# Kernel optimization log

Measured on AMD Instinct MI355X. Metric: run time of the kernel, lower is better.

## Reference

```python
import jax, jax.numpy as jnp
import numpy as np

D_EMB = 1024
N_HEADS = 16
HEAD_DIM = D_EMB // N_HEADS


def _xavier(key, out_f, in_f):
    limit = jnp.sqrt(6.0 / (in_f + out_f))
    return jax.random.uniform(key, (out_f, in_f), jnp.float32, -limit, limit)


def setup_inputs() -> dict:
    key = jax.random.key(0)
    k_x, k_qkv, k_out = jax.random.split(key, 3)
    x = jax.random.normal(k_x, (4, 2048, D_EMB), jnp.float32)
    # torch nn.Linear weights: [out_features, in_features], xavier_uniform; biases zero
    w_qkv = _xavier(k_qkv, 3 * D_EMB, D_EMB)
    b_qkv = jnp.zeros((3 * D_EMB,), jnp.float32)
    w_out = _xavier(k_out, D_EMB, D_EMB)
    b_out = jnp.zeros((D_EMB,), jnp.float32)
    return {"x": x, "w_qkv": w_qkv, "b_qkv": b_qkv, "w_out": w_out, "b_out": b_out}


def reference(x, w_qkv, b_qkv, w_out, b_out):
    B, S, D = x.shape
    # QKV projection: y = x @ W^T + b -> [B, S, 3D]
    qkv = jnp.einsum('bsd,ed->bse', x, w_qkv) + b_qkv
    # view(B, S, H, 3*head_dim) then split into q, k, v (matches torch chunk on last dim)
    qkv = qkv.reshape(B, S, N_HEADS, 3 * HEAD_DIM)
    q, k, v = jnp.split(qkv, 3, axis=-1)  # each [B, S, H, head_dim]
    scale = 1.0 / jnp.sqrt(jnp.float32(HEAD_DIM))
    scores = jnp.einsum('bshd,bthd->bhst', q, k) * scale  # [B, H, S, S]
    probs = jax.nn.softmax(scores, axis=-1)
    out = jnp.einsum('bhst,bthd->bshd', probs, v).reshape(B, S, D)
    return jnp.einsum('bsd,ed->bse', out, w_out) + b_out
```

## Files before the change

### kernel.cpp

```cpp
#include <hip/hip_runtime.h>

typedef __bf16 bf16_t;
typedef __bf16 bf16x8 __attribute__((ext_vector_type(8)));
typedef __bf16 bf16x4 __attribute__((ext_vector_type(4)));
typedef float f32x4 __attribute__((ext_vector_type(4)));

#define S_LEN 2048
#define D_EMB 1024
#define NH 16

#define MFMA16(a, b, c) __builtin_amdgcn_mfma_f32_16x16x32_bf16((a), (b), (c), 0, 0, 0)

__device__ __forceinline__ void gld16(void* lds, const void* g) {
  __builtin_amdgcn_global_load_lds(
      (__attribute__((address_space(1))) void*)(void*)(g),
      (__attribute__((address_space(3))) void*)(lds), 16, 0, 0);
}

__device__ __forceinline__ float exp2_hw(float x) {
  float r;
  asm("v_exp_f32 %0, %1" : "=v"(r) : "v"(x));
  return r;
}

__global__ __launch_bounds__(256) void cvt_bf16(const float* __restrict__ in,
                                                bf16_t* __restrict__ out, int n4) {
  int i = blockIdx.x * 256 + threadIdx.x;
  if (i >= n4) return;
  float4 v = ((const float4*)in)[i];
  bf16x4 o;
  o[0] = (bf16_t)v.x; o[1] = (bf16_t)v.y; o[2] = (bf16_t)v.z; o[3] = (bf16_t)v.w;
  ((bf16x4*)out)[i] = o;
}

template <int EPI>
__global__ __launch_bounds__(256) void gemm_bt(
    const bf16_t* __restrict__ A, const bf16_t* __restrict__ W,
    const float* __restrict__ bias, float* __restrict__ outF,
    bf16_t* __restrict__ outQ, int M, int N, int K) {
  __shared__ __attribute__((aligned(16))) bf16_t As[128 * 64];
  __shared__ __attribute__((aligned(16))) bf16_t Ws[128 * 64];
  const int tid = threadIdx.x;
  const int lane = tid & 63;
  const int wid = tid >> 6;
  const int l15 = lane & 15, lg = lane >> 4;
  int lin = blockIdx.x + gridDim.x * blockIdx.y;
  const int nwg = gridDim.x * gridDim.y;
  lin = (lin & 7) * (nwg >> 3) + (lin >> 3);
  const int tm = (lin / gridDim.x) * 128, tn = (lin % gridDim.x) * 128;
  const int wm = (wid >> 1) * 64, wn = (wid & 1) * 64;
  f32x4 acc[4][4] = {};
  const int q0 = tid * 16;

  for (int k0 = 0; k0 < K; k0 += 64) {
#pragma unroll
    for (int i = 0; i < 4; ++i) {
      int q = q0 + i * 4096;
      int row = q >> 7;
      int scb = (q & 127) ^ ((row & 7) << 4);
      gld16((char*)As + (q & ~1023),
            (const char*)A + ((size_t)(tm + row) * K + k0) * 2 + scb);
      gld16((char*)Ws + (q & ~1023),
            (const char*)W + ((size_t)(tn + row) * K + k0) * 2 + scb);
    }
    __syncthreads();
#pragma unroll
    for (int kk = 0; kk < 2; ++kk) {
      const int cb = kk * 64 + lg * 16;
      bf16x8 af[4], bfr[4];
#pragma unroll
      for (int mi = 0; mi < 4; ++mi) {
        int row = wm + mi * 16 + l15;
        af[mi] = *(const bf16x8*)((const char*)As + row * 128 + (cb ^ ((row & 7) << 4)));
      }
#pragma unroll
      for (int ni = 0; ni < 4; ++ni) {
        int row = wn + ni * 16 + l15;
        bfr[ni] = *(const bf16x8*)((const char*)Ws + row * 128 + (cb ^ ((row & 7) << 4)));
      }
#pragma unroll
      for (int mi = 0; mi < 4; ++mi)
#pragma unroll
        for (int ni = 0; ni < 4; ++ni)
          acc[mi][ni] = MFMA16(af[mi], bfr[ni], acc[mi][ni]);
    }
    __syncthreads();
  }

  if (EPI == 0) {
#pragma unroll
    for (int mi = 0; mi < 4; ++mi)
#pragma unroll
      for (int ni = 0; ni < 4; ++ni) {
        int colg = tn + wn + ni * 16 + l15;
        float bv = bias[colg];
#pragma unroll
        for (int j = 0; j < 4; ++j) {
          int rowg = tm + wm + mi * 16 + lg * 4 + j;
          outF[(size_t)rowg * N + colg] = acc[mi][ni][j] + bv;
        }
      }
  } else {
#pragma unroll
    for (int mi = 0; mi < 4; ++mi)
#pragma unroll
      for (int ni = 0; ni < 4; ++ni) {
        int e = tn + wn + ni * 16 + l15;
        float bv = bias[e];
        int h = e / 192;
        int r = e - h * 192;
        int t = r >> 6, c = r & 63;
#pragma unroll
        for (int j = 0; j < 4; ++j) {
          int m = tm + wm + mi * 16 + lg * 4 + j;
          int b = m >> 11, s = m & 2047;
          float v = acc[mi][ni][j] + bv;
          if (t == 0) v *= 0.18033688011112042f;
          size_t base = ((size_t)(b * NH + h) * 3 + t) * (size_t)(S_LEN * 64);
          size_t idx;
          if (t == 2) {
            int rs = s & 31;
            int rp = (((rs >> 2) & 3) << 3) | ((rs >> 4) << 2) | (rs & 3);
            idx = base + (size_t)c * S_LEN + (size_t)((s & ~31) | rp);
          } else {
            idx = base + (size_t)s * 64 + c;
          }
          outQ[idx] = (bf16_t)v;
        }
      }
  }
}

__global__ __launch_bounds__(256) void attn_fwd(const bf16_t* __restrict__ qkvb,
                                                bf16_t* __restrict__ attnb) {
  __shared__ __attribute__((aligned(16))) bf16_t Ks[2][64 * 64];
  __shared__ __attribute__((aligned(16))) bf16_t Vs[2][64 * 64];
  const int tid = threadIdx.x, lane = tid & 63, wid = tid >> 6;
  const int l15 = lane & 15, lg = lane >> 4;
  int lin = blockIdx.x + (blockIdx.y << 4);
  lin = (lin & 7) * 128 + (lin >> 3);
  const int qt = lin & 15;
  const int bh = lin >> 4;
  const int b = bh >> 4, h = bh & 15;
  const char* Qg = (const char*)qkvb + (size_t)bh * 3 * (S_LEN * 64) * 2;
  const char* Kg = Qg + (size_t)S_LEN * 64 * 2;
  const char* Vtg = Kg + (size_t)S_LEN * 64 * 2;
  const int q0 = tid * 16;

#pragma unroll
  for (int i = 0; i < 2; ++i) {
    int q = q0 + i * 4096;
    int row = q >> 7;
    int scb = (q & 127) ^ ((row & 7) << 4);
    gld16((char*)Ks[0] + (q & ~1023), Kg + (size_t)row * 128 + scb);
    gld16((char*)Vs[0] + (q & ~1023), Vtg + (size_t)row * (S_LEN * 2) + scb);
  }

  bf16x8 qf[2][2];
#pragma unroll
  for (int mi = 0; mi < 2; ++mi) {
    const char* qr = Qg + (size_t)(qt * 128 + wid * 32 + mi * 16 + l15) * 128;
#pragma unroll
    for (int kb = 0; kb < 2; ++kb)
      qf[mi][kb] = *(const bf16x8*)(qr + kb * 64 + lg * 16);
  }
  __syncthreads();

  float lsum[2] = {0.f, 0.f};
  f32x4 o[2][4] = {};
  const int swk = (l15 & 7) << 4;

  for (int kt = 0; kt < 32; ++kt) {
    const int cur = kt & 1;
    if (kt < 31) {
#pragma unroll
      for (int i = 0; i < 2; ++i) {
        int q = q0 + i * 4096;
        int row = q >> 7;
        int scb = (q & 127) ^ ((row & 7) << 4);
        gld16((char*)Ks[cur ^ 1] + (q & ~1023),
              Kg + (size_t)((kt + 1) * 64 + row) * 128 + scb);
        gld16((char*)Vs[cur ^ 1] + (q & ~1023),
              Vtg + (size_t)row * (S_LEN * 2) + (kt + 1) * 128 + scb);
      }
    }

    f32x4 stv[2][4];
#pragma unroll
    for (int nk = 0; nk < 4; ++nk) {
      const char* kr = (const char*)Ks[cur] + (nk * 16 + l15) * 128;
      bf16x8 kf0 = *(const bf16x8*)(kr + ((lg * 16) ^ swk));
      bf16x8 kf1 = *(const bf16x8*)(kr + ((64 + lg * 16) ^ swk));
#pragma unroll
      for (int mi = 0; mi < 2; ++mi) {
        f32x4 z = {};
        z = MFMA16(kf0, qf[mi][0], z);
        stv[mi][nk] = MFMA16(kf1, qf[mi][1], z);
      }
    }

#pragma unroll
    for (int mi = 0; mi < 2; ++mi)
#pragma unroll
      for (int nk = 0; nk < 4; ++nk)
#pragma unroll
        for (int j = 0; j < 4; ++j) {
          float p = exp2_hw(stv[mi][nk][j]);
          stv[mi][nk][j] = p;
          lsum[mi] += p;
        }

#pragma unroll
    for (int kp = 0; kp < 2; ++kp) {
      bf16x8 pf[2];
#pragma unroll
      for (int mi = 0; mi < 2; ++mi)
#pragma unroll
        for (int j = 0; j < 4; ++j) {
          pf[mi][j] = (bf16_t)stv[mi][2 * kp][j];
          pf[mi][4 + j] = (bf16_t)stv[mi][2 * kp + 1][j];
        }
#pragma unroll
      for (int ndv = 0; ndv < 4; ++ndv) {
        const char* vr = (const char*)Vs[cur] + (ndv * 16 + l15) * 128;
        bf16x8 vf = *(const bf16x8*)(vr + ((kp * 64 + 16 * lg) ^ swk));
        o[0][ndv] = MFMA16(pf[0], vf, o[0][ndv]);
        o[1][ndv] = MFMA16(pf[1], vf, o[1][ndv]);
      }
    }

    if (kt < 31) __syncthreads();
  }

#pragma unroll
  for (int mi = 0; mi < 2; ++mi) {
    lsum[mi] += __shfl_xor(lsum[mi], 16);
    lsum[mi] += __shfl_xor(lsum[mi], 32);
  }
  float inv[2][4];
#pragma unroll
  for (int mi = 0; mi < 2; ++mi)
#pragma unroll
    for (int j = 0; j < 4; ++j)
      inv[mi][j] = 1.0f / __shfl(lsum[mi], (lane & 48) | (lg * 4 + j));

#pragma unroll
  for (int mi = 0; mi < 2; ++mi)
#pragma unroll
    for (int j = 0; j < 4; ++j) {
      int srow = qt * 128 + wid * 32 + mi * 16 + lg * 4 + j;
      bf16_t* dst = attnb + ((size_t)b * S_LEN + srow) * D_EMB + h * 64;
#pragma unroll
      for (int ndv = 0; ndv < 4; ++ndv)
        dst[ndv * 16 + l15] = (bf16_t)(o[mi][ndv][j] * inv[mi][j]);
    }
}

extern "C" void kernel_launch(void* const* d_in, const int* in_sizes, int n_in,
                              void* d_out, int out_size, void* d_ws, size_t ws_size,
                              hipStream_t stream) {
  const float* x = (const float*)d_in[0];
  const float* w_qkv = (const float*)d_in[1];
  const float* b_qkv = (const float*)d_in[2];
  const float* w_out = (const float*)d_in[3];
  const float* b_out = (const float*)d_in[4];
  float* out = (float*)d_out;

  bf16_t* xb = (bf16_t*)d_ws;
  bf16_t* wqkvb = xb + 8388608;
  bf16_t* woutb = wqkvb + 3145728;
  bf16_t* qkvb = woutb + 1048576;
  bf16_t* attnb = qkvb + 25165824;

  cvt_bf16<<<8192, 256, 0, stream>>>(x, xb, 2097152);
  cvt_bf16<<<3072, 256, 0, stream>>>(w_qkv, wqkvb, 786432);
  cvt_bf16<<<1024, 256, 0, stream>>>(w_out, woutb, 262144);

  gemm_bt<1><<<dim3(24, 64), 256, 0, stream>>>(xb, wqkvb, b_qkv, nullptr, qkvb,
                                               8192, 3072, 1024);
  attn_fwd<<<dim3(16, 64), 256, 0, stream>>>(qkvb, attnb);
  gemm_bt<0><<<dim3(8, 64), 256, 0, stream>>>(attnb, woutb, b_out, out, nullptr,
                                              8192, 1024, 1024);
}
```

Measured before the change: 212.4 us.

## Triple-buffer K/V tiles in attention with prefetch depth two and vmcnt waits

```diff
diff --git a/kernel.cpp b/kernel.cpp
--- a/kernel.cpp
+++ b/kernel.cpp
@@ -133,8 +133,8 @@
 
 __global__ __launch_bounds__(256) void attn_fwd(const bf16_t* __restrict__ qkvb,
                                                 bf16_t* __restrict__ attnb) {
-  __shared__ __attribute__((aligned(16))) bf16_t Ks[2][64 * 64];
-  __shared__ __attribute__((aligned(16))) bf16_t Vs[2][64 * 64];
+  __shared__ __attribute__((aligned(16))) bf16_t Ks[3][64 * 64];
+  __shared__ __attribute__((aligned(16))) bf16_t Vs[3][64 * 64];
   const int tid = threadIdx.x, lane = tid & 63, wid = tid >> 6;
   const int l15 = lane & 15, lg = lane >> 4;
   int lin = blockIdx.x + (blockIdx.y << 4);
@@ -147,15 +147,6 @@
   const char* Vtg = Kg + (size_t)S_LEN * 64 * 2;
   const int q0 = tid * 16;
 
-#pragma unroll
-  for (int i = 0; i < 2; ++i) {
-    int q = q0 + i * 4096;
-    int row = q >> 7;
-    int scb = (q & 127) ^ ((row & 7) << 4);
-    gld16((char*)Ks[0] + (q & ~1023), Kg + (size_t)row * 128 + scb);
-    gld16((char*)Vs[0] + (q & ~1023), Vtg + (size_t)row * (S_LEN * 2) + scb);
-  }
-
   bf16x8 qf[2][2];
 #pragma unroll
   for (int mi = 0; mi < 2; ++mi) {
@@ -164,31 +155,43 @@
     for (int kb = 0; kb < 2; ++kb)
       qf[mi][kb] = *(const bf16x8*)(qr + kb * 64 + lg * 16);
   }
-  __syncthreads();
+
+  auto stage = [&](int t) {
+#pragma unroll
+    for (int i = 0; i < 2; ++i) {
+      int q = q0 + i * 4096;
+      int row = q >> 7;
+      int scb = (q & 127) ^ ((row & 7) << 4);
+      gld16((char*)Ks[t % 3] + (q & ~1023),
+            Kg + (size_t)(t * 64 + row) * 128 + scb);
+      gld16((char*)Vs[t % 3] + (q & ~1023),
+            Vtg + (size_t)row * (S_LEN * 2) + t * 128 + scb);
+    }
+  };
+  stage(0);
+  stage(1);
 
   float lsum[2] = {0.f, 0.f};
   f32x4 o[2][4] = {};
   const int swk = (l15 & 7) << 4;
 
   for (int kt = 0; kt < 32; ++kt) {
-    const int cur = kt & 1;
     if (kt < 31) {
-#pragma unroll
-      for (int i = 0; i < 2; ++i) {
-        int q = q0 + i * 4096;
-        int row = q >> 7;
-        int scb = (q & 127) ^ ((row & 7) << 4);
-        gld16((char*)Ks[cur ^ 1] + (q & ~1023),
-              Kg + (size_t)((kt + 1) * 64 + row) * 128 + scb);
-        gld16((char*)Vs[cur ^ 1] + (q & ~1023),
-              Vtg + (size_t)row * (S_LEN * 2) + (kt + 1) * 128 + scb);
-      }
-    }
+      asm volatile("s_waitcnt vmcnt(4)" ::: "memory");
+    } else {
+      asm volatile("s_waitcnt vmcnt(0)" ::: "memory");
+    }
+    __builtin_amdgcn_s_barrier();
+    asm volatile("" ::: "memory");
+    if (kt + 2 < 32) stage(kt + 2);
+
+    const bf16_t* Kc = Ks[kt % 3];
+    const bf16_t* Vc = Vs[kt % 3];
 
     f32x4 stv[2][4];
 #pragma unroll
     for (int nk = 0; nk < 4; ++nk) {
-      const char* kr = (const char*)Ks[cur] + (nk * 16 + l15) * 128;
+      const char* kr = (const char*)Kc + (nk * 16 + l15) * 128;
       bf16x8 kf0 = *(const bf16x8*)(kr + ((lg * 16) ^ swk));
       bf16x8 kf1 = *(const bf16x8*)(kr + ((64 + lg * 16) ^ swk));
 #pragma unroll
@@ -222,14 +225,12 @@
         }
 #pragma unroll
       for (int ndv = 0; ndv < 4; ++ndv) {
-        const char* vr = (const char*)Vs[cur] + (ndv * 16 + l15) * 128;
+        const char* vr = (const char*)Vc + (ndv * 16 + l15) * 128;
         bf16x8 vf = *(const bf16x8*)(vr + ((kp * 64 + 16 * lg) ^ swk));
         o[0][ndv] = MFMA16(pf[0], vf, o[0][ndv]);
         o[1][ndv] = MFMA16(pf[1], vf, o[1][ndv]);
       }
     }
-
-    if (kt < 31) __syncthreads();
   }
 
 #pragma unroll
```

After: 212.2 us. Within noise of the previous version (-0.1%).
